# Kernel tuning notes

Hardware: AMD Instinct MI355X
Metric: run time of the kernel (lower is better)

## Reference

```python
import jax, jax.numpy as jnp
import numpy as np

EPS = 1e-12
N_NODES = 100000
N_EDGES = 1600000
IN_CH = 8
N_CLASSES = 16
MAX_ORDER = 1
N_RINGS = 2


def setup_inputs() -> dict:
    key = jax.random.key(0)
    k0, k1, k2, k3, k4 = jax.random.split(key, 5)
    x = jax.random.normal(k0, (N_NODES, IN_CH), dtype=jnp.float32)
    edge_index = jax.random.randint(k1, (2, N_EDGES), 0, N_NODES)
    precomp = jax.random.normal(k2, (N_EDGES, MAX_ORDER + 1, N_RINGS, 2), dtype=jnp.float32)
    connection = jax.random.normal(k3, (N_EDGES, 2), dtype=jnp.float32)
    # n_orders = (prev_order+1)*(max_order+1) with default prev_order=1 -> 2*(max_order+1)
    n_orders = 2 * (MAX_ORDER + 1)
    radial_profile = jax.random.normal(k4, (n_orders, N_RINGS, N_CLASSES, IN_CH), dtype=jnp.float32) * 0.1
    bias = jnp.zeros((N_CLASSES,), dtype=jnp.float32)
    return dict(x=x, edge_index=edge_index, precomp=precomp,
                connection=connection, radial_profile=radial_profile, bias=bias)


def reference(x, edge_index, precomp, connection, radial_profile, bias):
    # x is stacked with zeros -> complex features with a single stream (M=1, input_order=0).
    # Since input_order==0 only, `connection` (parallel transport) is never applied.
    N = x.shape[0]
    O1 = MAX_ORDER + 1
    src = edge_index[0]  # aggregation targets (flow='target_to_source')
    tgt = edge_index[1]  # gathered neighbours (x_j)
    xjr = x[tgt]                      # [E, F] real part
    xji = jnp.zeros_like(xjr)         # [E, F] imaginary part (zeros by construction)
    # m = |output_order - 0| = output_order; sign = np.sign(m) -> 0 for order 0, +1 otherwise
    signs = jnp.sign(jnp.arange(O1, dtype=x.dtype))
    pre_re = jnp.transpose(precomp[..., 0], (0, 2, 1))          # [E, R, O1]
    pre_im = jnp.transpose(precomp[..., 1], (0, 2, 1)) * signs  # [E, R, O1]
    a_re = xjr[:, None, :, None]      # [E, 1, F, 1]
    a_im = xji[:, None, :, None]
    b_re = pre_re[:, :, None, :]      # [E, R, 1, O1]
    b_im = pre_im[:, :, None, :]
    msg_re = a_re * b_re - a_im * b_im   # [E, R, F, O1]
    msg_im = a_re * b_im + a_im * b_re
    aggr_re = jax.ops.segment_sum(msg_re, src, num_segments=N)  # [N, R, F, O1]
    aggr_im = jax.ops.segment_sum(msg_im, src, num_segments=N)
    # update: m_idx = 0*(max_order+1)+output_order, offset=False
    prof = radial_profile[:O1]        # [O1, R, C, F]
    out_re = jnp.einsum('orcf,nrfo->noc', prof, aggr_re)  # [N, O1, C]
    out_im = jnp.einsum('orcf,nrfo->noc', prof, aggr_im)
    mag = jnp.sqrt(jnp.maximum(out_re * out_re + out_im * out_im, EPS))  # [N, O1, C]
    logits = mag.sum(axis=1) + bias   # [N, C]
    return jax.nn.log_softmax(logits, axis=1)
```

## Files before the change

### kernel.cpp

```cpp
#include <hip/hip_runtime.h>
#include <hip/hip_fp16.h>

#define N_NODES 100000
#define N_EDGES 1600000
#define IN_CH 8
#define N_CLASSES 16

#define NPB 64
#define NPB_SHIFT 6
#define NB ((N_NODES + NPB - 1) / NPB)
#define NB_PAD 1568
#define BIN_T 3125
#define NBLK 512
#define MAX_BE 1536

union H2I { __half2 h; int i; };

#define RECBUF_OFF  0
#define BCNT_OFF    ((size_t)N_EDGES * 16)
#define COLSUM_OFF  (BCNT_OFF + (size_t)NBLK * NB_PAD * 4)
#define GBASE_OFF   (COLSUM_OFF + (size_t)NB_PAD * 4)
#define BIN_WS_BYTES (GBASE_OFF + ((size_t)NB + 4) * 4)

#define AGGR_RE_FLOATS (N_NODES * 32)
#define AGGR_IM_FLOATS (N_NODES * 16)
#define WS_FLOATS (AGGR_RE_FLOATS + AGGR_IM_FLOATS)
#define WS_F4 (WS_FLOATS / 4)


__global__ __launch_bounds__(1024) void hist_kernel(const int* __restrict__ ei,
                                                    int* __restrict__ bcnt) {
    __shared__ int h[NB_PAD];
    int t = threadIdx.x;
    for (int i = t; i < NB_PAD; i += 1024) h[i] = 0;
    __syncthreads();
    int base = blockIdx.x * BIN_T;
    int end = base + BIN_T; if (end > N_EDGES) end = N_EDGES;
    for (int e = base + t; e < end; e += 1024)
        atomicAdd(&h[ei[e] >> NPB_SHIFT], 1);
    __syncthreads();
    for (int i = t; i < NB_PAD; i += 1024)
        bcnt[(size_t)blockIdx.x * NB_PAD + i] = h[i];
}

__global__ __launch_bounds__(1024) void colscan_kernel(int* __restrict__ bcnt,
                                                       int* __restrict__ colsum) {
    __shared__ int sbuf[16][65];
    int t = threadIdx.x;
    int r64 = t >> 4, c = t & 15;
    int c0 = blockIdx.x * 16;
    int vals[8];
    int partial = 0;
#pragma unroll
    for (int k = 0; k < 8; ++k) {
        int row = r64 * 8 + k;
        int v = bcnt[(size_t)row * NB_PAD + c0 + c];
        vals[k] = v;
        partial += v;
    }
    sbuf[c][r64] = partial;
    __syncthreads();
#pragma unroll
    for (int d = 1; d < 64; d <<= 1) {
        int u = (r64 >= d) ? sbuf[c][r64 - d] : 0;
        __syncthreads();
        sbuf[c][r64] += u;
        __syncthreads();
    }
    int running = sbuf[c][r64] - partial;
#pragma unroll
    for (int k = 0; k < 8; ++k) {
        int row = r64 * 8 + k;
        bcnt[(size_t)row * NB_PAD + c0 + c] = running;
        running += vals[k];
    }
    if (r64 == 63) colsum[c0 + c] = sbuf[c][63];
}

__global__ __launch_bounds__(1024) void base_kernel(const int* __restrict__ colsum,
                                                    int* __restrict__ gbase) {
    __shared__ int buf[1024];
    int t = threadIdx.x;
    int i0 = 2 * t, i1 = 2 * t + 1;
    int v0 = (i0 < NB) ? colsum[i0] : 0;
    int v1 = (i1 < NB) ? colsum[i1] : 0;
    buf[t] = v0 + v1;
    __syncthreads();
#pragma unroll
    for (int d = 1; d < 1024; d <<= 1) {
        int u = (t >= d) ? buf[t - d] : 0;
        __syncthreads();
        buf[t] += u;
        __syncthreads();
    }
    int excl = buf[t] - (v0 + v1);
    if (i0 < NB) gbase[i0] = excl;
    if (i1 < NB) gbase[i1] = excl + v0;
    if (t == 1023) gbase[NB] = buf[1023];
}

__global__ __launch_bounds__(1024) void bin_kernel(
    const int* __restrict__ ei, const float* __restrict__ precomp,
    const int* __restrict__ bcnt, const int* __restrict__ gbase,
    int4* __restrict__ recbuf) {
    __shared__ int lbase[NB];
    __shared__ int lcnt[NB];
    int t = threadIdx.x;
    for (int i = t; i < NB; i += 1024) {
        lbase[i] = gbase[i] + bcnt[(size_t)blockIdx.x * NB_PAD + i];
        lcnt[i] = 0;
    }
    __syncthreads();
    int base = blockIdx.x * BIN_T;
    int end = base + BIN_T; if (end > N_EDGES) end = N_EDGES;
    for (int e = base + t; e < end; e += 1024) {
        int src = ei[e];
        int tgt = ei[N_EDGES + e];
        int b = src >> NPB_SHIFT;
        int rank = atomicAdd(&lcnt[b], 1);
        size_t pos = (size_t)(lbase[b] + rank);
        const float4* pc = (const float4*)(precomp + (size_t)e * 8);
        float4 q0 = pc[0], q1 = pc[1];
        H2I u0, u1, u2;
        u0.h = __floats2half2_rn(q0.x, q0.z);
        u1.h = __floats2half2_rn(q1.x, q1.y);
        u2.h = __floats2half2_rn(q1.z, q1.w);
        int packed = tgt | ((src & (NPB - 1)) << 17);
        recbuf[pos] = make_int4(u0.i, u1.i, u2.i, packed);
    }
}

__global__ __launch_bounds__(512) void aggregate_kernel(
    const int* __restrict__ gbase, const int4* __restrict__ recbuf,
    const float* __restrict__ x,
    const float* __restrict__ prof, const float* __restrict__ bias,
    float* __restrict__ out) {
    __shared__ float sprof[512];
    __shared__ int cnt[NPB];
    __shared__ int start[NPB];
    __shared__ int cur[NPB];
    __shared__ int skey[MAX_BE];
    __shared__ int srec[MAX_BE];
    __shared__ float acc[NPB * 48];

    int t = threadIdx.x, b = blockIdx.x;
    sprof[t] = prof[t];
    if (t < NPB) cnt[t] = 0;
    __syncthreads();

    int lo = gbase[b], hi = gbase[b + 1];
    int n = hi - lo; if (n > MAX_BE) n = MAX_BE;
    const int* ri = (const int*)recbuf;

    for (int k = t; k < n; k += 512) {
        int key = ri[(size_t)(lo + k) * 4 + 3];
        skey[k] = key;
        atomicAdd(&cnt[((unsigned)key) >> 17], 1);
    }
    __syncthreads();

    if (t < 64) {
        int v = cnt[t];
        int s = v;
#pragma unroll
        for (int d = 1; d < 64; d <<= 1) {
            int u = __shfl_up(s, d, 64);
            if (t >= d) s += u;
        }
        start[t] = s - v;
        cur[t] = s - v;
    }
    __syncthreads();

    for (int k = t; k < n; k += 512) {
        int packed = skey[k];
        int nl = ((unsigned)packed) >> 17;
        int p = atomicAdd(&cur[nl], 1);
        srec[p] = (packed & 0x1FFFF) | (k << 17);
    }
    __syncthreads();

    int nl = t >> 3, f = t & 7;
    float a0r0 = 0.f, a1r0 = 0.f, aIr0 = 0.f, a0r1 = 0.f, a1r1 = 0.f, aIr1 = 0.f;
    int s0 = start[nl], n0 = cnt[nl];
    for (int k = 0; k < n0; ++k) {
        int rec = srec[s0 + k];
        int slot = ((unsigned)rec) >> 17;
        int tgt = rec & 0x1FFFF;
        int4 rv = recbuf[(size_t)(lo + slot)];
        H2I u0, u1, u2; u0.i = rv.x; u1.i = rv.y; u2.i = rv.z;
        float2 f0 = __half22float2(u0.h);
        float2 f1 = __half22float2(u1.h);
        float2 f2 = __half22float2(u2.h);
        float xv = x[tgt * IN_CH + f];
        a0r0 = fmaf(xv, f0.x, a0r0);
        a0r1 = fmaf(xv, f0.y, a0r1);
        a1r0 = fmaf(xv, f1.x, a1r0);
        aIr0 = fmaf(xv, f1.y, aIr0);
        a1r1 = fmaf(xv, f2.x, a1r1);
        aIr1 = fmaf(xv, f2.y, aIr1);
    }
    float* a = acc + nl * 48;
    a[f * 3 + 0] = a0r0;  a[f * 3 + 1] = a1r0;  a[f * 3 + 2] = aIr0;
    a[24 + f * 3 + 0] = a0r1;  a[24 + f * 3 + 1] = a1r1;  a[24 + f * 3 + 2] = aIr1;
    __syncthreads();

#pragma unroll
    for (int pass = 0; pass < 2; ++pass) {
        int nl2 = pass * 32 + (t >> 4);
        int c = t & 15;
        int gnode = b * NPB + nl2;
        if (gnode < N_NODES) {
            float re0 = 0.f, re1 = 0.f, im1 = 0.f;
#pragma unroll
            for (int rr = 0; rr < 2; ++rr) {
#pragma unroll
                for (int ff = 0; ff < 8; ++ff) {
                    int idx = nl2 * 48 + rr * 24 + ff * 3;
                    float w0 = sprof[(0 * 2 + rr) * 128 + c * 8 + ff];
                    float w1 = sprof[(1 * 2 + rr) * 128 + c * 8 + ff];
                    re0 = fmaf(w0, acc[idx + 0], re0);
                    re1 = fmaf(w1, acc[idx + 1], re1);
                    im1 = fmaf(w1, acc[idx + 2], im1);
                }
            }
            float mag = sqrtf(fmaxf(re0 * re0, 1e-12f)) +
                        sqrtf(fmaxf(re1 * re1 + im1 * im1, 1e-12f));
            float logit = mag + bias[c];
            float m = logit;
#pragma unroll
            for (int o = 1; o < 16; o <<= 1) m = fmaxf(m, __shfl_xor(m, o, 16));
            float ex = __expf(logit - m);
            float s = ex;
#pragma unroll
            for (int o = 1; o < 16; o <<= 1) s += __shfl_xor(s, o, 16);
            out[gnode * N_CLASSES + c] = (logit - m) - logf(s);
        }
    }
}


__global__ __launch_bounds__(256) void zero_ws_kernel(float4* __restrict__ ws, int n4) {
    int i = blockIdx.x * blockDim.x + threadIdx.x;
    if (i < n4) ws[i] = make_float4(0.f, 0.f, 0.f, 0.f);
}

__global__ __launch_bounds__(256) void edge_kernel(
    const int* __restrict__ ei, const float* __restrict__ x,
    const float* __restrict__ precomp,
    float* __restrict__ aggrRe, float* __restrict__ aggrIm) {
    int gid = blockIdx.x * blockDim.x + threadIdx.x;
    int e = gid >> 3;
    int f = gid & 7;
    if (e >= N_EDGES) return;
    int src = ei[e];
    int tgt = ei[N_EDGES + e];
    float xv = x[tgt * IN_CH + f];
    const float4* pc = (const float4*)(precomp + (size_t)e * 8);
    float4 p0 = pc[0], p1 = pc[1];
    float* ar = aggrRe + (size_t)src * 32;
    atomicAdd(ar + ((0 * 8 + f) * 2 + 0), xv * p0.x);
    atomicAdd(ar + ((1 * 8 + f) * 2 + 0), xv * p0.z);
    atomicAdd(ar + ((0 * 8 + f) * 2 + 1), xv * p1.x);
    atomicAdd(ar + ((1 * 8 + f) * 2 + 1), xv * p1.z);
    float* ai = aggrIm + (size_t)src * 16;
    atomicAdd(ai + (0 * 8 + f), xv * p1.y);
    atomicAdd(ai + (1 * 8 + f), xv * p1.w);
}

__global__ __launch_bounds__(256) void node_kernel(
    const float* __restrict__ aggrRe, const float* __restrict__ aggrIm,
    const float* __restrict__ prof, const float* __restrict__ bias,
    float* __restrict__ out) {
    __shared__ float sprof[512];
    for (int i = threadIdx.x; i < 512; i += blockDim.x) sprof[i] = prof[i];
    __syncthreads();
    int gid = blockIdx.x * blockDim.x + threadIdx.x;
    int n = gid >> 4;
    int c = gid & 15;
    if (n >= N_NODES) return;
    const float* ar = aggrRe + (size_t)n * 32;
    const float* ai = aggrIm + (size_t)n * 16;
    float re0 = 0.f, re1 = 0.f, im1 = 0.f;
#pragma unroll
    for (int r = 0; r < 2; ++r)
#pragma unroll
        for (int f = 0; f < 8; ++f) {
            float a0 = ar[(r * 8 + f) * 2 + 0];
            float a1 = ar[(r * 8 + f) * 2 + 1];
            float aI = ai[r * 8 + f];
            float w0 = sprof[(0 * 2 + r) * 128 + c * 8 + f];
            float w1 = sprof[(1 * 2 + r) * 128 + c * 8 + f];
            re0 = fmaf(w0, a0, re0);
            re1 = fmaf(w1, a1, re1);
            im1 = fmaf(w1, aI, im1);
        }
    float mag = sqrtf(fmaxf(re0 * re0, 1e-12f)) +
                sqrtf(fmaxf(re1 * re1 + im1 * im1, 1e-12f));
    float logit = mag + bias[c];
    float m = logit;
#pragma unroll
    for (int o = 1; o < 16; o <<= 1) m = fmaxf(m, __shfl_xor(m, o, 16));
    float ex = __expf(logit - m);
    float s = ex;
#pragma unroll
    for (int o = 1; o < 16; o <<= 1) s += __shfl_xor(s, o, 16);
    out[n * N_CLASSES + c] = (logit - m) - logf(s);
}


extern "C" void kernel_launch(void* const* d_in, const int* in_sizes, int n_in,
                              void* d_out, int out_size, void* d_ws, size_t ws_size,
                              hipStream_t stream) {
    const float* x       = (const float*)d_in[0];
    const int*   ei      = (const int*)d_in[1];
    const float* precomp = (const float*)d_in[2];
    const float* prof    = (const float*)d_in[4];
    const float* bias    = (const float*)d_in[5];
    float* out = (float*)d_out;

    if (ws_size >= BIN_WS_BYTES) {
        char* ws = (char*)d_ws;
        int4* recbuf = (int4*)(ws + RECBUF_OFF);
        int* bcnt    = (int*)(ws + BCNT_OFF);
        int* colsum  = (int*)(ws + COLSUM_OFF);
        int* gbase   = (int*)(ws + GBASE_OFF);

        hist_kernel<<<NBLK, 1024, 0, stream>>>(ei, bcnt);
        colscan_kernel<<<NB_PAD / 16, 1024, 0, stream>>>(bcnt, colsum);
        base_kernel<<<1, 1024, 0, stream>>>(colsum, gbase);
        bin_kernel<<<NBLK, 1024, 0, stream>>>(ei, precomp, bcnt, gbase, recbuf);
        aggregate_kernel<<<NB, 512, 0, stream>>>(gbase, recbuf, x, prof, bias, out);
    } else {
        float* aggrRe = (float*)d_ws;
        float* aggrIm = aggrRe + AGGR_RE_FLOATS;
        zero_ws_kernel<<<(WS_F4 + 255) / 256, 256, 0, stream>>>((float4*)d_ws, WS_F4);
        int edge_threads = N_EDGES * 8;
        edge_kernel<<<(edge_threads + 255) / 256, 256, 0, stream>>>(ei, x, precomp, aggrRe, aggrIm);
        int node_threads = N_NODES * 16;
        node_kernel<<<(node_threads + 255) / 256, 256, 0, stream>>>(aggrRe, aggrIm, prof, bias, out);
    }
}
```

Baseline: 75.39 us.

## Replace global histogram and scans with per-tile local binning in two kernels

Removes the hist, column-scan and base-scan kernels. Each bin block now does its own local histogram and scan, then writes records into its own tile region along with a transposed per-tile bucket start table. The aggregate kernel scans the 512 per-tile counts for its bucket, gathers the records directly into shared memory and sorts them there by node, so it never rereads recbuf from global. This cuts three launches and the global scan traffic. In exchange each aggregate block gathers from 512 scattered small segments with a serial per-thread copy loop.

```diff
diff --git a/kernel.cpp b/kernel.cpp
--- a/kernel.cpp
+++ b/kernel.cpp
@@ -9,18 +9,15 @@
 #define NPB 64
 #define NPB_SHIFT 6
 #define NB ((N_NODES + NPB - 1) / NPB)
-#define NB_PAD 1568
 #define BIN_T 3125
 #define NBLK 512
 #define MAX_BE 1536
 
 union H2I { __half2 h; int i; };
 
-#define RECBUF_OFF  0
-#define BCNT_OFF    ((size_t)N_EDGES * 16)
-#define COLSUM_OFF  (BCNT_OFF + (size_t)NBLK * NB_PAD * 4)
-#define GBASE_OFF   (COLSUM_OFF + (size_t)NB_PAD * 4)
-#define BIN_WS_BYTES (GBASE_OFF + ((size_t)NB + 4) * 4)
+#define RECBUF_OFF   0
+#define TSTART_OFF   ((size_t)N_EDGES * 16)
+#define BIN_WS_BYTES (TSTART_OFF + (size_t)(NB + 1) * NBLK * 2)
 
 #define AGGR_RE_FLOATS (N_NODES * 32)
 #define AGGR_IM_FLOATS (N_NODES * 16)
@@ -28,97 +25,54 @@
 #define WS_F4 (WS_FLOATS / 4)
 
 
-__global__ __launch_bounds__(1024) void hist_kernel(const int* __restrict__ ei,
-                                                    int* __restrict__ bcnt) {
-    __shared__ int h[NB_PAD];
-    int t = threadIdx.x;
-    for (int i = t; i < NB_PAD; i += 1024) h[i] = 0;
-    __syncthreads();
-    int base = blockIdx.x * BIN_T;
-    int end = base + BIN_T; if (end > N_EDGES) end = N_EDGES;
-    for (int e = base + t; e < end; e += 1024)
-        atomicAdd(&h[ei[e] >> NPB_SHIFT], 1);
-    __syncthreads();
-    for (int i = t; i < NB_PAD; i += 1024)
-        bcnt[(size_t)blockIdx.x * NB_PAD + i] = h[i];
-}
-
-__global__ __launch_bounds__(1024) void colscan_kernel(int* __restrict__ bcnt,
-                                                       int* __restrict__ colsum) {
-    __shared__ int sbuf[16][65];
-    int t = threadIdx.x;
-    int r64 = t >> 4, c = t & 15;
-    int c0 = blockIdx.x * 16;
-    int vals[8];
-    int partial = 0;
-#pragma unroll
-    for (int k = 0; k < 8; ++k) {
-        int row = r64 * 8 + k;
-        int v = bcnt[(size_t)row * NB_PAD + c0 + c];
-        vals[k] = v;
-        partial += v;
-    }
-    sbuf[c][r64] = partial;
-    __syncthreads();
-#pragma unroll
-    for (int d = 1; d < 64; d <<= 1) {
-        int u = (r64 >= d) ? sbuf[c][r64 - d] : 0;
-        __syncthreads();
-        sbuf[c][r64] += u;
-        __syncthreads();
-    }
-    int running = sbuf[c][r64] - partial;
-#pragma unroll
-    for (int k = 0; k < 8; ++k) {
-        int row = r64 * 8 + k;
-        bcnt[(size_t)row * NB_PAD + c0 + c] = running;
-        running += vals[k];
-    }
-    if (r64 == 63) colsum[c0 + c] = sbuf[c][63];
-}
-
-__global__ __launch_bounds__(1024) void base_kernel(const int* __restrict__ colsum,
-                                                    int* __restrict__ gbase) {
-    __shared__ int buf[1024];
-    int t = threadIdx.x;
-    int i0 = 2 * t, i1 = 2 * t + 1;
-    int v0 = (i0 < NB) ? colsum[i0] : 0;
-    int v1 = (i1 < NB) ? colsum[i1] : 0;
-    buf[t] = v0 + v1;
-    __syncthreads();
-#pragma unroll
-    for (int d = 1; d < 1024; d <<= 1) {
-        int u = (t >= d) ? buf[t - d] : 0;
-        __syncthreads();
-        buf[t] += u;
-        __syncthreads();
-    }
-    int excl = buf[t] - (v0 + v1);
-    if (i0 < NB) gbase[i0] = excl;
-    if (i1 < NB) gbase[i1] = excl + v0;
-    if (t == 1023) gbase[NB] = buf[1023];
-}
-
 __global__ __launch_bounds__(1024) void bin_kernel(
     const int* __restrict__ ei, const float* __restrict__ precomp,
-    const int* __restrict__ bcnt, const int* __restrict__ gbase,
-    int4* __restrict__ recbuf) {
-    __shared__ int lbase[NB];
+    int4* __restrict__ recbuf, unsigned short* __restrict__ tstartT) {
     __shared__ int lcnt[NB];
+    __shared__ int tst[NB];
+    __shared__ int sscan[1024];
+
     int t = threadIdx.x;
+    int tile = blockIdx.x;
+    int base = tile * BIN_T;
+
+    for (int i = t; i < NB; i += 1024) lcnt[i] = 0;
+    __syncthreads();
+
+    for (int e = base + t; e < base + BIN_T; e += 1024)
+        atomicAdd(&lcnt[ei[e] >> NPB_SHIFT], 1);
+    __syncthreads();
+
+    int i0 = 2 * t, i1 = 2 * t + 1;
+    int v0 = (i0 < NB) ? lcnt[i0] : 0;
+    int v1 = (i1 < NB) ? lcnt[i1] : 0;
+    sscan[t] = v0 + v1;
+    __syncthreads();
+#pragma unroll
+    for (int d = 1; d < 1024; d <<= 1) {
+        int u = (t >= d) ? sscan[t - d] : 0;
+        __syncthreads();
+        sscan[t] += u;
+        __syncthreads();
+    }
+    int excl = sscan[t] - (v0 + v1);
+    if (i0 < NB) tst[i0] = excl;
+    if (i1 < NB) tst[i1] = excl + v0;
+    __syncthreads();
+
     for (int i = t; i < NB; i += 1024) {
-        lbase[i] = gbase[i] + bcnt[(size_t)blockIdx.x * NB_PAD + i];
+        tstartT[(size_t)i * NBLK + tile] = (unsigned short)tst[i];
         lcnt[i] = 0;
     }
-    __syncthreads();
-    int base = blockIdx.x * BIN_T;
-    int end = base + BIN_T; if (end > N_EDGES) end = N_EDGES;
-    for (int e = base + t; e < end; e += 1024) {
+    if (t == 0) tstartT[(size_t)NB * NBLK + tile] = (unsigned short)BIN_T;
+    __syncthreads();
+
+    for (int e = base + t; e < base + BIN_T; e += 1024) {
         int src = ei[e];
         int tgt = ei[N_EDGES + e];
         int b = src >> NPB_SHIFT;
         int rank = atomicAdd(&lcnt[b], 1);
-        size_t pos = (size_t)(lbase[b] + rank);
+        int s = tst[b] + rank;
         const float4* pc = (const float4*)(precomp + (size_t)e * 8);
         float4 q0 = pc[0], q1 = pc[1];
         H2I u0, u1, u2;
@@ -126,36 +80,53 @@
         u1.h = __floats2half2_rn(q1.x, q1.y);
         u2.h = __floats2half2_rn(q1.z, q1.w);
         int packed = tgt | ((src & (NPB - 1)) << 17);
-        recbuf[pos] = make_int4(u0.i, u1.i, u2.i, packed);
+        recbuf[(size_t)base + s] = make_int4(u0.i, u1.i, u2.i, packed);
     }
 }
 
 __global__ __launch_bounds__(512) void aggregate_kernel(
-    const int* __restrict__ gbase, const int4* __restrict__ recbuf,
+    const int4* __restrict__ recbuf, const unsigned short* __restrict__ tstartT,
     const float* __restrict__ x,
     const float* __restrict__ prof, const float* __restrict__ bias,
     float* __restrict__ out) {
     __shared__ float sprof[512];
+    __shared__ int4 srec16[MAX_BE];
+    __shared__ int srt[MAX_BE];
     __shared__ int cnt[NPB];
     __shared__ int start[NPB];
     __shared__ int cur[NPB];
-    __shared__ int skey[MAX_BE];
-    __shared__ int srec[MAX_BE];
+    __shared__ int sscan[512];
     __shared__ float acc[NPB * 48];
+    __shared__ int ntot;
 
     int t = threadIdx.x, b = blockIdx.x;
     sprof[t] = prof[t];
     if (t < NPB) cnt[t] = 0;
-    __syncthreads();
-
-    int lo = gbase[b], hi = gbase[b + 1];
-    int n = hi - lo; if (n > MAX_BE) n = MAX_BE;
-    const int* ri = (const int*)recbuf;
-
-    for (int k = t; k < n; k += 512) {
-        int key = ri[(size_t)(lo + k) * 4 + 3];
-        skey[k] = key;
-        atomicAdd(&cnt[((unsigned)key) >> 17], 1);
+
+    int st = (int)tstartT[(size_t)b * NBLK + t];
+    int en = (int)tstartT[(size_t)(b + 1) * NBLK + t];
+    int cn = en - st;
+    sscan[t] = cn;
+    __syncthreads();
+#pragma unroll
+    for (int d = 1; d < 512; d <<= 1) {
+        int u = (t >= d) ? sscan[t - d] : 0;
+        __syncthreads();
+        sscan[t] += u;
+        __syncthreads();
+    }
+    int ofs = sscan[t] - cn;
+    if (t == 511) ntot = sscan[511] < MAX_BE ? sscan[511] : MAX_BE;
+    __syncthreads();
+    int n = ntot;
+
+    for (int k = 0; k < cn; ++k) {
+        int p = ofs + k;
+        if (p < MAX_BE) {
+            int4 rv = recbuf[(size_t)t * BIN_T + st + k];
+            srec16[p] = rv;
+            atomicAdd(&cnt[((unsigned)rv.w) >> 17], 1);
+        }
     }
     __syncthreads();
 
@@ -173,10 +144,10 @@
     __syncthreads();
 
     for (int k = t; k < n; k += 512) {
-        int packed = skey[k];
-        int nl = ((unsigned)packed) >> 17;
+        int key = srec16[k].w;
+        int nl = ((unsigned)key) >> 17;
         int p = atomicAdd(&cur[nl], 1);
-        srec[p] = (packed & 0x1FFFF) | (k << 17);
+        srt[p] = (key & 0x1FFFF) | (k << 17);
     }
     __syncthreads();
 
@@ -184,10 +155,10 @@
     float a0r0 = 0.f, a1r0 = 0.f, aIr0 = 0.f, a0r1 = 0.f, a1r1 = 0.f, aIr1 = 0.f;
     int s0 = start[nl], n0 = cnt[nl];
     for (int k = 0; k < n0; ++k) {
-        int rec = srec[s0 + k];
+        int rec = srt[s0 + k];
         int slot = ((unsigned)rec) >> 17;
         int tgt = rec & 0x1FFFF;
-        int4 rv = recbuf[(size_t)(lo + slot)];
+        int4 rv = srec16[slot];
         H2I u0, u1, u2; u0.i = rv.x; u1.i = rv.y; u2.i = rv.z;
         float2 f0 = __half22float2(u0.h);
         float2 f1 = __half22float2(u1.h);
@@ -321,16 +292,11 @@
 
     if (ws_size >= BIN_WS_BYTES) {
         char* ws = (char*)d_ws;
-        int4* recbuf = (int4*)(ws + RECBUF_OFF);
-        int* bcnt    = (int*)(ws + BCNT_OFF);
-        int* colsum  = (int*)(ws + COLSUM_OFF);
-        int* gbase   = (int*)(ws + GBASE_OFF);
-
-        hist_kernel<<<NBLK, 1024, 0, stream>>>(ei, bcnt);
-        colscan_kernel<<<NB_PAD / 16, 1024, 0, stream>>>(bcnt, colsum);
-        base_kernel<<<1, 1024, 0, stream>>>(colsum, gbase);
-        bin_kernel<<<NBLK, 1024, 0, stream>>>(ei, precomp, bcnt, gbase, recbuf);
-        aggregate_kernel<<<NB, 512, 0, stream>>>(gbase, recbuf, x, prof, bias, out);
+        int4* recbuf            = (int4*)(ws + RECBUF_OFF);
+        unsigned short* tstartT = (unsigned short*)(ws + TSTART_OFF);
+
+        bin_kernel<<<NBLK, 1024, 0, stream>>>(ei, precomp, recbuf, tstartT);
+        aggregate_kernel<<<NB, 512, 0, stream>>>(recbuf, tstartT, x, prof, bias, out);
     } else {
         float* aggrRe = (float*)d_ws;
         float* aggrIm = aggrRe + AGGR_RE_FLOATS;
```

Result: slower. 82.02 us (+8.8%).
